# Kernel optimization log

Hardware: AMD Instinct MI355X
Metric: run time of the kernel (lower is better)

The kernel has to match this reference:

```python
import jax, jax.numpy as jnp
import numpy as np

C = 768  # in_channel == out_channel (required by conv9)

def _conv1x1(x, w, b):
    # x: [B,C,H,W], w: [O,C], b: [O]
    return jnp.einsum('bchw,oc->bohw', x, w) + b[None, :, None, None]

def _rot(x):
    # torch: gather with reversed index along dim 3, then permute(0,1,3,2)
    return jnp.swapaxes(jnp.flip(x, axis=3), 2, 3)

def _forward(hidden_states, Ws, bs):
    x = hidden_states
    B, Cc, W, H = x.shape
    o1 = _rot(x); o2 = _rot(o1); o3 = _rot(o2)
    hs11 = (jax.nn.relu(_conv1x1(x,  Ws[0], bs[0]))
          + jax.nn.relu(_conv1x1(o1, Ws[1], bs[1]))
          + jax.nn.relu(_conv1x1(o2, Ws[2], bs[2]))
          + jax.nn.relu(_conv1x1(o3, Ws[3], bs[3])))
    s = W // 2
    e1 = x[:, :, 0:s, 0:s]; e2 = x[:, :, 0:s, s:W]
    e3 = x[:, :, s:W, 0:s]; e4 = x[:, :, s:W, s:W]
    quads = [e1, e2, e3, e4]
    ts = []
    for _ in range(3):
        quads = [_rot(q) for q in quads]
        top = jnp.concatenate((quads[0], quads[1]), axis=-1)
        bot = jnp.concatenate((quads[2], quads[3]), axis=-1)
        ts.append(jnp.concatenate((top, bot), axis=-2))
    hs111 = (jax.nn.relu(_conv1x1(x,     Ws[4], bs[4]))
           + jax.nn.relu(_conv1x1(ts[0], Ws[5], bs[5]))
           + jax.nn.relu(_conv1x1(ts[1], Ws[6], bs[6]))
           + jax.nn.relu(_conv1x1(ts[2], Ws[7], bs[7])))
    # --- spatial matmul attention (per batch & channel, over HxW) ---
    q, k, v = hs11, hs111, hs11
    att = jnp.einsum('bcik,bckj->bcij', q, k)        # [B,C,W,W]
    attn = jax.nn.softmax(att, axis=-1)               # dropout = identity (eval)
    out = jnp.einsum('bcij,bcjh->bcih', attn, v)      # [B,C,W,H]
    out = jax.nn.relu(_conv1x1(out, Ws[8], bs[8]))    # proj dropout = identity (eval)
    return out

def setup_inputs() -> dict:
    key = jax.random.key(0)
    k1, k2, k3 = jax.random.split(key, 3)
    hidden_states = jax.random.normal(k1, (32, C, 32, 32), dtype=jnp.float32)
    # 9 Conv2d(C, C, kernel_size=1) layers -> stacked [9, O, C] weights and [9, O] biases
    fan_in = C
    bound = 1.0 / np.sqrt(fan_in)
    Ws = jax.random.uniform(k2, (9, C, C), minval=-bound, maxval=bound, dtype=jnp.float32)
    bs = jax.random.uniform(k3, (9, C), minval=-bound, maxval=bound, dtype=jnp.float32)
    return {"hidden_states": hidden_states, "Ws": Ws, "bs": bs}

def reference(hidden_states, Ws, bs):
    return _forward(hidden_states, Ws, bs)
```

## Files before the change

### kernel.cpp

```cpp
#include <hip/hip_runtime.h>
#include <hip/hip_fp16.h>

typedef unsigned short u16;
typedef unsigned int u32;
typedef float f32x4 __attribute__((ext_vector_type(4)));
typedef _Float16 half8 __attribute__((ext_vector_type(8)));
typedef unsigned short u16x4 __attribute__((ext_vector_type(4)));

#define CDIM 768
#define NP 1024
#define NB 32

static constexpr size_t CHW = (size_t)NB * CDIM * NP;

static constexpr size_t XT_OFF  = 0;
static constexpr size_t HS_OFF  = CHW * 2;
static constexpr size_t WHI_OFF = HS_OFF + CHW * 4;

__device__ __forceinline__ u16 f16bits(float f) {
  return __half_as_ushort(__float2half_rn(f));
}
__device__ __forceinline__ float f16tof(u16 b) {
  __half_raw hr; hr.x = b; return __half2float(__half(hr));
}
__device__ __forceinline__ u32 pk2(u32 p, float a, float b) {
  float x = f16tof((u16)(p & 0xffff)) + a;
  float y = f16tof((u16)(p >> 16)) + b;
  return (u32)f16bits(x) | ((u32)f16bits(y) << 16);
}

typedef __attribute__((address_space(1))) void gv_t;
typedef __attribute__((address_space(3))) void lv_t;
__device__ __forceinline__ void gload_lds16(const void* g, void* l) {
  __builtin_amdgcn_global_load_lds((gv_t*)g, (lv_t*)l, 16, 0, 0);
}

__global__ __launch_bounds__(256) void cast_w_k(const float* __restrict__ W,
                                                u16* __restrict__ hi) {
  int i = blockIdx.x * 256 + threadIdx.x;
  float4 v = ((const float4*)W)[i];
  u16x4 h4 = {f16bits(v.x), f16bits(v.y), f16bits(v.z), f16bits(v.w)};
  ((u16x4*)hi)[i] = h4;
}

__global__ __launch_bounds__(256) void transpose_f16_k(const float* __restrict__ src,
                                                       u16* __restrict__ dxt) {
  __shared__ float tle[32][33];
  const int b = blockIdx.z, c0 = blockIdx.y * 32, p0 = blockIdx.x * 32;
  const int tid = threadIdx.x;
  const int lr = tid >> 5, lc = tid & 31;
  const float* s = src + ((size_t)b * CDIM + c0) * NP + p0;
#pragma unroll
  for (int it = 0; it < 4; ++it) {
    int c = it * 8 + lr;
    tle[c][lc] = s[(size_t)c * NP + lc];
  }
  __syncthreads();
#pragma unroll
  for (int it = 0; it < 4; ++it) {
    int p = it * 8 + lr;
    float v = tle[lc][p];
    size_t off = ((size_t)b * NP + p0 + p) * CDIM + c0 + lc;
    dxt[off] = f16bits(v);
  }
}

__device__ __forceinline__ int sigma_fn(int mode, int z, int t, int p) {
  if (t == 0 || mode == 1) return p;
  int i = p >> 5, j = p & 31;
  if (z == 0) {
    if (t == 1) return (j << 5) | (31 - i);
    if (t == 2) return ((31 - i) << 5) | (31 - j);
    return ((31 - j) << 5) | i;
  } else {
    int ib = i & 16, jb = j & 16, il = i & 15, jl = j & 15;
    if (t == 1) return ((ib | jl) << 5) | (jb | (15 - il));
    if (t == 2) return ((ib | (15 - il)) << 5) | (jb | (15 - jl));
    return ((ib | (15 - jl)) << 5) | (jb | il);
  }
}

template <int OUTF16, int NTERMS>
__global__ __launch_bounds__(512, 2) void gemm_r(
    const u16* __restrict__ Whi,
    const u16* __restrict__ Bx,
    const float* __restrict__ bias, void* __restrict__ dst,
    int wselBase, int mode) {
  extern __shared__ u16 lds[];
  const int tid = threadIdx.x;
  const int lane = tid & 63;
  const int w = tid >> 6;
  const int wr = w >> 2, wc = w & 3;
  const int z = blockIdx.z;
  const int b = blockIdx.x >> 2;
  const int p0 = (blockIdx.x & 3) << 8;
  const int o0 = blockIdx.y << 8;
  const int l15 = lane & 15, l4 = lane >> 4;
  float* blds = (float*)(lds + 49152);
  const int NSTEP = NTERMS * 24;

  const int rA = wr * 128 + l15;
  const int baseA = rA * 32 + (l4 ^ ((rA >> 1) & 3)) * 8;
  const int rB = wc * 64 + l15;
  const int baseB = 8192 + rB * 32 + (l4 ^ ((rB >> 1) & 3)) * 8;

  int srow[2], scof[2];
#pragma unroll
  for (int it = 0; it < 2; ++it) {
    int d = it * 512 + tid;
    srow[it] = d >> 2;
    scof[it] = ((d & 3) ^ ((srow[it] >> 1) & 3)) * 8;
  }
  const u16* aptr[2];
  const u16* bptr[2];
  auto setPtrs = [&](int term) {
    int wsel = wselBase + z * 4 + term;
#pragma unroll
    for (int it = 0; it < 2; ++it) {
      aptr[it] = Whi + ((size_t)wsel * CDIM + o0 + srow[it]) * CDIM + scof[it];
      int srw = sigma_fn(mode, z, term, p0 + srow[it]);
      bptr[it] = Bx + ((size_t)b * NP + srw) * CDIM + scof[it];
    }
  };
  auto stageA = [&](u16* ldst) {
    gload_lds16(aptr[0], ldst + tid * 8);
    gload_lds16(aptr[1], ldst + 4096 + tid * 8);
    aptr[0] += 32; aptr[1] += 32;
  };
  auto stageB = [&](u16* ldst) {
    gload_lds16(bptr[0], ldst + 8192 + tid * 8);
    gload_lds16(bptr[1], ldst + 12288 + tid * 8);
    bptr[0] += 32; bptr[1] += 32;
  };

  for (int i = tid; i < NTERMS * 256; i += 512)
    blds[i] = bias[(size_t)(wselBase + z * 4 + (i >> 8)) * CDIM + o0 + (i & 255)];
  asm volatile("s_waitcnt lgkmcnt(0)" ::: "memory");

  f32x4 acc[8][4];
#pragma unroll
  for (int mi = 0; mi < 8; ++mi)
#pragma unroll
    for (int ni = 0; ni < 4; ++ni) acc[mi][ni] = (f32x4){0.f, 0.f, 0.f, 0.f};
  u32 rp[8][4][2];
  if (NTERMS > 1) {
#pragma unroll
    for (int mi = 0; mi < 8; ++mi)
#pragma unroll
      for (int ni = 0; ni < 4; ++ni) { rp[mi][ni][0] = 0u; rp[mi][ni][1] = 0u; }
  }

  setPtrs(0);
  stageA(lds); stageB(lds);
  stageA(lds + 16384); stageB(lds + 16384);

  int nsk = 2, nst = 0;
  int ckk = 0, cterm = 0;
  int cur = 0, wb = 2;

  for (int s = 0; s < NSTEP; ++s) {
    if (s + 1 < NSTEP) {
      asm volatile("s_waitcnt vmcnt(4)" ::: "memory");
    } else {
      asm volatile("s_waitcnt vmcnt(0)" ::: "memory");
    }
    __builtin_amdgcn_s_barrier();
    asm volatile("" ::: "memory");

    const u16* la = lds + cur * 16384;
    u16* ldst = lds + wb * 16384;
    const bool dostage = (s + 2) < NSTEP;
    if (dostage && nsk == 24) { ++nst; nsk = 0; setPtrs(nst); }

    half8 af[4], bf[4];
#pragma unroll
    for (int n = 0; n < 4; ++n) bf[n] = *(const half8*)(la + baseB + n * 512);
#pragma unroll
    for (int m = 0; m < 4; ++m) af[m] = *(const half8*)(la + baseA + m * 512);
    if (dostage) stageA(ldst);
    asm volatile("s_waitcnt lgkmcnt(0)" ::: "memory");
    __builtin_amdgcn_s_setprio(1);
#pragma unroll
    for (int m = 0; m < 4; ++m)
#pragma unroll
      for (int n = 0; n < 4; ++n)
        acc[m][n] = __builtin_amdgcn_mfma_f32_16x16x32_f16(af[m], bf[n], acc[m][n], 0, 0, 0);
    __builtin_amdgcn_s_setprio(0);

#pragma unroll
    for (int m = 0; m < 4; ++m) af[m] = *(const half8*)(la + baseA + (4 + m) * 512);
    if (dostage) { stageB(ldst); ++nsk; }
    asm volatile("s_waitcnt lgkmcnt(0)" ::: "memory");
    __builtin_amdgcn_s_setprio(1);
#pragma unroll
    for (int m = 0; m < 4; ++m)
#pragma unroll
      for (int n = 0; n < 4; ++n)
        acc[4 + m][n] = __builtin_amdgcn_mfma_f32_16x16x32_f16(af[m], bf[n], acc[4 + m][n], 0, 0, 0);
    __builtin_amdgcn_s_setprio(0);

    if (NTERMS > 1 && ckk == 23) {
#pragma unroll
      for (int mi = 0; mi < 8; ++mi) {
        float4 bv = *(const float4*)&blds[cterm * 256 + wr * 128 + mi * 16 + l4 * 4];
#pragma unroll
        for (int ni = 0; ni < 4; ++ni) {
          rp[mi][ni][0] = pk2(rp[mi][ni][0], fmaxf(0.f, acc[mi][ni][0] + bv.x),
                                             fmaxf(0.f, acc[mi][ni][1] + bv.y));
          rp[mi][ni][1] = pk2(rp[mi][ni][1], fmaxf(0.f, acc[mi][ni][2] + bv.z),
                                             fmaxf(0.f, acc[mi][ni][3] + bv.w));
          acc[mi][ni] = (f32x4){0.f, 0.f, 0.f, 0.f};
        }
      }
    }
    cur = cur == 2 ? 0 : cur + 1;
    wb = wb == 2 ? 0 : wb + 1;
    ++ckk; if (ckk == 24) { ckk = 0; ++cterm; }
  }

#pragma unroll
  for (int mi = 0; mi < 8; ++mi) {
    int rowb = o0 + wr * 128 + mi * 16 + l4 * 4;
#pragma unroll
    for (int ni = 0; ni < 4; ++ni) {
      int col = p0 + wc * 64 + ni * 16 + l15;
      size_t base = ((size_t)b * CDIM + rowb) * NP + col;
      if (NTERMS > 1) {
        u16* dp = (u16*)dst + (size_t)z * CHW + base;
        dp[0 * NP] = (u16)(rp[mi][ni][0] & 0xffff);
        dp[1 * NP] = (u16)(rp[mi][ni][0] >> 16);
        dp[2 * NP] = (u16)(rp[mi][ni][1] & 0xffff);
        dp[3 * NP] = (u16)(rp[mi][ni][1] >> 16);
      } else {
        float4 bv = *(const float4*)&blds[wr * 128 + mi * 16 + l4 * 4];
        float bvf[4] = {bv.x, bv.y, bv.z, bv.w};
        float* dp = (float*)dst + (size_t)z * CHW + base;
#pragma unroll
        for (int r = 0; r < 4; ++r)
          dp[(size_t)r * NP] = fmaxf(0.f, acc[mi][ni][r] + bvf[r]);
      }
    }
  }
}

__global__ __launch_bounds__(256) void attn_m_k(const u16* __restrict__ hs, u16* __restrict__ aoT) {
  __shared__ float q[4][1024];
  __shared__ float kk[4][1024];
  const int tid = threadIdx.x, w = tid >> 6, lane = tid & 63;
  const int pair0 = blockIdx.x * 4;
  const int b = pair0 / CDIM;
  const int c0 = pair0 % CDIM;
  const int l15 = lane & 15, l4 = lane >> 4;

#pragma unroll
  for (int it = 0; it < 8; ++it) {
    int d4 = it * 256 + tid;
    int pr = d4 >> 9;
    int mat = (d4 >> 8) & 1;
    int off4 = d4 & 255;
    ushort4 hv = *(const ushort4*)&hs[(size_t)mat * CHW + (size_t)(pair0 + pr) * NP + off4 * 4];
    float* dl = mat ? kk[pr] : q[pr];
    int off = off4 * 4;
    int row = off >> 5;
    int ph = ((off & 31) >> 2) ^ (row & 7) ^ (row >> 3);
    float4 v = {f16tof(hv.x), f16tof(hv.y), f16tof(hv.z), f16tof(hv.w)};
    *(float4*)&dl[row * 32 + ph * 4] = v;
  }
  __syncthreads();

  const float* Q = q[w];
  float* KK = kk[w];

  auto rd_row8 = [&](const float* M, int row) -> half8 {
    int rx = (row & 7) ^ (row >> 3);
    float4 a = *(const float4*)&M[row * 32 + ((2 * l4) ^ rx) * 4];
    float4 c = *(const float4*)&M[row * 32 + ((2 * l4 + 1) ^ rx) * 4];
    half8 h;
    h[0] = (_Float16)a.x; h[1] = (_Float16)a.y; h[2] = (_Float16)a.z; h[3] = (_Float16)a.w;
    h[4] = (_Float16)c.x; h[5] = (_Float16)c.y; h[6] = (_Float16)c.z; h[7] = (_Float16)c.w;
    return h;
  };
  auto rd_col8 = [&](const float* M, int col) -> half8 {
    half8 h;
#pragma unroll
    for (int e = 0; e < 8; ++e) {
      int row = l4 * 8 + e;
      int ph = (col >> 2) ^ (row & 7) ^ (row >> 3);
      h[e] = (_Float16)M[row * 32 + ph * 4 + (col & 3)];
    }
    return h;
  };

  half8 bq[2], akk[2];
#pragma unroll
  for (int it = 0; it < 2; ++it) bq[it] = rd_row8(Q, it * 16 + l15);
#pragma unroll
  for (int mh = 0; mh < 2; ++mh) akk[mh] = rd_col8(KK, mh * 16 + l15);
  f32x4 sacc[2][2];
#pragma unroll
  for (int mh = 0; mh < 2; ++mh)
#pragma unroll
    for (int it = 0; it < 2; ++it)
      sacc[mh][it] = __builtin_amdgcn_mfma_f32_16x16x32_f16(
          akk[mh], bq[it], (f32x4){0.f, 0.f, 0.f, 0.f}, 0, 0, 0);

#pragma unroll
  for (int it = 0; it < 2; ++it) {
    float mx = sacc[0][it][0];
#pragma unroll
    for (int r = 1; r < 4; ++r) mx = fmaxf(mx, sacc[0][it][r]);
#pragma unroll
    for (int r = 0; r < 4; ++r) mx = fmaxf(mx, sacc[1][it][r]);
    mx = fmaxf(mx, __shfl_xor(mx, 16));
    mx = fmaxf(mx, __shfl_xor(mx, 32));
    float pv[2][4];
    float sum = 0.f;
#pragma unroll
    for (int mh = 0; mh < 2; ++mh)
#pragma unroll
      for (int r = 0; r < 4; ++r) {
        pv[mh][r] = expf(sacc[mh][it][r] - mx);
        sum += pv[mh][r];
      }
    sum += __shfl_xor(sum, 16);
    sum += __shfl_xor(sum, 32);
    float inv = 1.f / sum;
    int row = it * 16 + l15;
    int rx = (row & 7) ^ (row >> 3);
#pragma unroll
    for (int mh = 0; mh < 2; ++mh) {
      float4 v = {pv[mh][0] * inv, pv[mh][1] * inv, pv[mh][2] * inv, pv[mh][3] * inv};
      *(float4*)&KK[row * 32 + ((mh * 4 + l4) ^ rx) * 4] = v;
    }
  }

  half8 bp[2], av[2];
#pragma unroll
  for (int it = 0; it < 2; ++it) bp[it] = rd_row8(KK, it * 16 + l15);
#pragma unroll
  for (int ht = 0; ht < 2; ++ht) av[ht] = rd_col8(Q, ht * 16 + l15);
  f32x4 oacc[2][2];
#pragma unroll
  for (int ht = 0; ht < 2; ++ht)
#pragma unroll
    for (int it = 0; it < 2; ++it)
      oacc[ht][it] = __builtin_amdgcn_mfma_f32_16x16x32_f16(
          av[ht], bp[it], (f32x4){0.f, 0.f, 0.f, 0.f}, 0, 0, 0);

#pragma unroll
  for (int it = 0; it < 2; ++it) {
    int row = it * 16 + l15;
    int rx = (row & 7) ^ (row >> 3);
#pragma unroll
    for (int ht = 0; ht < 2; ++ht) {
      float4 v = {oacc[ht][it][0], oacc[ht][it][1], oacc[ht][it][2], oacc[ht][it][3]};
      *(float4*)&KK[row * 32 + ((ht * 4 + l4) ^ rx) * 4] = v;
    }
  }
  __syncthreads();

#pragma unroll
  for (int it = 0; it < 4; ++it) {
    int p = it * 256 + tid;
    int row = p >> 5, col = p & 31;
    int idx = row * 32 + (((col >> 2) ^ (row & 7) ^ (row >> 3)) * 4) + (col & 3);
    ushort4 v;
    v.x = f16bits(kk[0][idx]);
    v.y = f16bits(kk[1][idx]);
    v.z = f16bits(kk[2][idx]);
    v.w = f16bits(kk[3][idx]);
    *(ushort4*)&aoT[((size_t)b * NP + p) * CDIM + c0] = v;
  }
}

extern "C" void kernel_launch(void* const* d_in, const int* in_sizes, int n_in,
                              void* d_out, int out_size, void* d_ws, size_t ws_size,
                              hipStream_t stream) {
  (void)in_sizes; (void)n_in; (void)out_size; (void)ws_size;
  const float* x = (const float*)d_in[0];
  const float* Ws = (const float*)d_in[1];
  const float* bs = (const float*)d_in[2];
  float* out = (float*)d_out;
  char* ws = (char*)d_ws;

  u16* XT  = (u16*)(ws + XT_OFF);
  u16* hs  = (u16*)(ws + HS_OFF);
  u16* Whi = (u16*)(ws + WHI_OFF);
  u16* aoT = (u16*)(ws + XT_OFF);

  cast_w_k<<<5184, 256, 0, stream>>>(Ws, Whi);
  transpose_f16_k<<<dim3(32, 24, 32), 256, 0, stream>>>(x, XT);
  gemm_r<1, 4><<<dim3(128, 3, 2), 512, 102400, stream>>>(Whi, XT, bs, (void*)hs, 0, 0);
  attn_m_k<<<6144, 256, 0, stream>>>(hs, aoT);
  gemm_r<0, 1><<<dim3(128, 3, 1), 512, 99328, stream>>>(Whi, aoT, bs, (void*)out, 8, 1);
}
```

Measured before the change: 503.9 us.

## Tile attention output layout, split GEMM main loop into four phases, store attention in f16

The attention kernel now processes 16 channel pairs per 1024-thread block. It loads Q/K directly into LDS as f16 through global_load_lds with an XOR swizzle, keeps the intermediates in f16, and writes its output in a 16-channel tiled layout. The final projection GEMM reads that tiled layout through a new template flag, giving contiguous B loads. The GEMM main loop is also split into four MFMA sub-phases, each with its own barrier and a single staged async load, to interleave copies with compute. The extra barriers per k-step could add synchronization stalls.

```diff
diff --git a/kernel.cpp b/kernel.cpp
--- a/kernel.cpp
+++ b/kernel.cpp
@@ -11,7 +11,8 @@
 #define NP 1024
 #define NB 32
 
-static constexpr size_t CHW = (size_t)NB * CDIM * NP;
+static constexpr size_t PBATCH = (size_t)CDIM * NP;
+static constexpr size_t CHW = (size_t)NB * PBATCH;
 
 static constexpr size_t XT_OFF  = 0;
 static constexpr size_t HS_OFF  = CHW * 2;
@@ -23,6 +24,7 @@
 __device__ __forceinline__ float f16tof(u16 b) {
   __half_raw hr; hr.x = b; return __half2float(__half(hr));
 }
+__device__ __forceinline__ int akey(int r) { return ((r >> 1) & 3) ^ ((r >> 3) & 3); }
 __device__ __forceinline__ u32 pk2(u32 p, float a, float b) {
   float x = f16tof((u16)(p & 0xffff)) + a;
   float y = f16tof((u16)(p >> 16)) + b;
@@ -80,8 +82,8 @@
   }
 }
 
-template <int OUTF16, int NTERMS>
-__global__ __launch_bounds__(512, 2) void gemm_r(
+template <int OUTF16, int NTERMS, int TILEDB>
+__global__ __launch_bounds__(512, 2) void gemm_q8(
     const u16* __restrict__ Whi,
     const u16* __restrict__ Bx,
     const float* __restrict__ bias, void* __restrict__ dst,
@@ -118,19 +120,20 @@
 #pragma unroll
     for (int it = 0; it < 2; ++it) {
       aptr[it] = Whi + ((size_t)wsel * CDIM + o0 + srow[it]) * CDIM + scof[it];
-      int srw = sigma_fn(mode, z, term, p0 + srow[it]);
-      bptr[it] = Bx + ((size_t)b * NP + srw) * CDIM + scof[it];
+      if (TILEDB) {
+        int cc = scof[it];
+        bptr[it] = Bx + (size_t)b * PBATCH + (size_t)(cc >> 4) * (NP * 16) +
+                   (size_t)(p0 + srow[it]) * 16 + (cc & 15);
+      } else {
+        int srw = sigma_fn(mode, z, term, p0 + srow[it]);
+        bptr[it] = Bx + ((size_t)b * NP + srw) * CDIM + scof[it];
+      }
     }
   };
-  auto stageA = [&](u16* ldst) {
-    gload_lds16(aptr[0], ldst + tid * 8);
-    gload_lds16(aptr[1], ldst + 4096 + tid * 8);
+  auto advPtrs = [&]() {
     aptr[0] += 32; aptr[1] += 32;
-  };
-  auto stageB = [&](u16* ldst) {
-    gload_lds16(bptr[0], ldst + 8192 + tid * 8);
-    gload_lds16(bptr[1], ldst + 12288 + tid * 8);
-    bptr[0] += 32; bptr[1] += 32;
+    if (TILEDB) { bptr[0] += 32768; bptr[1] += 32768; }
+    else { bptr[0] += 32; bptr[1] += 32; }
   };
 
   for (int i = tid; i < NTERMS * 256; i += 512)
@@ -151,8 +154,16 @@
   }
 
   setPtrs(0);
-  stageA(lds); stageB(lds);
-  stageA(lds + 16384); stageB(lds + 16384);
+  gload_lds16(aptr[0], lds + tid * 8);
+  gload_lds16(aptr[1], lds + 4096 + tid * 8);
+  gload_lds16(bptr[0], lds + 8192 + tid * 8);
+  gload_lds16(bptr[1], lds + 12288 + tid * 8);
+  advPtrs();
+  gload_lds16(aptr[0], lds + 16384 + tid * 8);
+  gload_lds16(aptr[1], lds + 16384 + 4096 + tid * 8);
+  gload_lds16(bptr[0], lds + 16384 + 8192 + tid * 8);
+  gload_lds16(bptr[1], lds + 16384 + 12288 + tid * 8);
+  advPtrs();
 
   int nsk = 2, nst = 0;
   int ckk = 0, cterm = 0;
@@ -170,33 +181,65 @@
     const u16* la = lds + cur * 16384;
     u16* ldst = lds + wb * 16384;
     const bool dostage = (s + 2) < NSTEP;
-    if (dostage && nsk == 24) { ++nst; nsk = 0; setPtrs(nst); }
-
-    half8 af[4], bf[4];
+    if (NTERMS > 1 && dostage && nsk == 24) { ++nst; nsk = 0; setPtrs(nst); }
+
+    half8 bf[4], af[2];
 #pragma unroll
     for (int n = 0; n < 4; ++n) bf[n] = *(const half8*)(la + baseB + n * 512);
-#pragma unroll
-    for (int m = 0; m < 4; ++m) af[m] = *(const half8*)(la + baseA + m * 512);
-    if (dostage) stageA(ldst);
+    af[0] = *(const half8*)(la + baseA);
+    af[1] = *(const half8*)(la + baseA + 512);
+    if (dostage) gload_lds16(aptr[0], ldst + tid * 8);
+    __builtin_amdgcn_s_barrier();
     asm volatile("s_waitcnt lgkmcnt(0)" ::: "memory");
     __builtin_amdgcn_s_setprio(1);
 #pragma unroll
-    for (int m = 0; m < 4; ++m)
-#pragma unroll
-      for (int n = 0; n < 4; ++n)
-        acc[m][n] = __builtin_amdgcn_mfma_f32_16x16x32_f16(af[m], bf[n], acc[m][n], 0, 0, 0);
+    for (int n = 0; n < 4; ++n) {
+      acc[0][n] = __builtin_amdgcn_mfma_f32_16x16x32_f16(af[0], bf[n], acc[0][n], 0, 0, 0);
+      acc[1][n] = __builtin_amdgcn_mfma_f32_16x16x32_f16(af[1], bf[n], acc[1][n], 0, 0, 0);
+    }
     __builtin_amdgcn_s_setprio(0);
 
-#pragma unroll
-    for (int m = 0; m < 4; ++m) af[m] = *(const half8*)(la + baseA + (4 + m) * 512);
-    if (dostage) { stageB(ldst); ++nsk; }
+    af[0] = *(const half8*)(la + baseA + 2 * 512);
+    af[1] = *(const half8*)(la + baseA + 3 * 512);
+    if (dostage) gload_lds16(aptr[1], ldst + 4096 + tid * 8);
+    __builtin_amdgcn_s_barrier();
     asm volatile("s_waitcnt lgkmcnt(0)" ::: "memory");
     __builtin_amdgcn_s_setprio(1);
 #pragma unroll
-    for (int m = 0; m < 4; ++m)
-#pragma unroll
-      for (int n = 0; n < 4; ++n)
-        acc[4 + m][n] = __builtin_amdgcn_mfma_f32_16x16x32_f16(af[m], bf[n], acc[4 + m][n], 0, 0, 0);
+    for (int n = 0; n < 4; ++n) {
+      acc[2][n] = __builtin_amdgcn_mfma_f32_16x16x32_f16(af[0], bf[n], acc[2][n], 0, 0, 0);
+      acc[3][n] = __builtin_amdgcn_mfma_f32_16x16x32_f16(af[1], bf[n], acc[3][n], 0, 0, 0);
+    }
+    __builtin_amdgcn_s_setprio(0);
+
+    af[0] = *(const half8*)(la + baseA + 4 * 512);
+    af[1] = *(const half8*)(la + baseA + 5 * 512);
+    if (dostage) gload_lds16(bptr[0], ldst + 8192 + tid * 8);
+    __builtin_amdgcn_s_barrier();
+    asm volatile("s_waitcnt lgkmcnt(0)" ::: "memory");
+    __builtin_amdgcn_s_setprio(1);
+#pragma unroll
+    for (int n = 0; n < 4; ++n) {
+      acc[4][n] = __builtin_amdgcn_mfma_f32_16x16x32_f16(af[0], bf[n], acc[4][n], 0, 0, 0);
+      acc[5][n] = __builtin_amdgcn_mfma_f32_16x16x32_f16(af[1], bf[n], acc[5][n], 0, 0, 0);
+    }
+    __builtin_amdgcn_s_setprio(0);
+
+    af[0] = *(const half8*)(la + baseA + 6 * 512);
+    af[1] = *(const half8*)(la + baseA + 7 * 512);
+    if (dostage) {
+      gload_lds16(bptr[1], ldst + 12288 + tid * 8);
+      advPtrs();
+      ++nsk;
+    }
+    __builtin_amdgcn_s_barrier();
+    asm volatile("s_waitcnt lgkmcnt(0)" ::: "memory");
+    __builtin_amdgcn_s_setprio(1);
+#pragma unroll
+    for (int n = 0; n < 4; ++n) {
+      acc[6][n] = __builtin_amdgcn_mfma_f32_16x16x32_f16(af[0], bf[n], acc[6][n], 0, 0, 0);
+      acc[7][n] = __builtin_amdgcn_mfma_f32_16x16x32_f16(af[1], bf[n], acc[7][n], 0, 0, 0);
+    }
     __builtin_amdgcn_s_setprio(0);
 
     if (NTERMS > 1 && ckk == 23) {
@@ -243,59 +286,47 @@
   }
 }
 
-__global__ __launch_bounds__(256) void attn_m_k(const u16* __restrict__ hs, u16* __restrict__ aoT) {
-  __shared__ float q[4][1024];
-  __shared__ float kk[4][1024];
+__global__ __launch_bounds__(1024) void attn_t_k(const u16* __restrict__ hs, u16* __restrict__ aoT) {
+  extern __shared__ u16 att[];
   const int tid = threadIdx.x, w = tid >> 6, lane = tid & 63;
-  const int pair0 = blockIdx.x * 4;
+  const int pair0 = blockIdx.x * 16;
   const int b = pair0 / CDIM;
   const int c0 = pair0 % CDIM;
   const int l15 = lane & 15, l4 = lane >> 4;
 
 #pragma unroll
-  for (int it = 0; it < 8; ++it) {
-    int d4 = it * 256 + tid;
-    int pr = d4 >> 9;
-    int mat = (d4 >> 8) & 1;
-    int off4 = d4 & 255;
-    ushort4 hv = *(const ushort4*)&hs[(size_t)mat * CHW + (size_t)(pair0 + pr) * NP + off4 * 4];
-    float* dl = mat ? kk[pr] : q[pr];
-    int off = off4 * 4;
-    int row = off >> 5;
-    int ph = ((off & 31) >> 2) ^ (row & 7) ^ (row >> 3);
-    float4 v = {f16tof(hv.x), f16tof(hv.y), f16tof(hv.z), f16tof(hv.w)};
-    *(float4*)&dl[row * 32 + ph * 4] = v;
-  }
+  for (int it = 0; it < 4; ++it) {
+    int d = it * 1024 + tid;
+    int pair = d >> 8, mat = (d >> 7) & 1, rem = d & 127;
+    int r = rem >> 2, ph = rem & 3;
+    int ch = ph ^ akey(r);
+    const u16* src = hs + (size_t)mat * CHW + (size_t)(pair0 + pair) * NP + r * 32 + ch * 8;
+    gload_lds16(src, att + (size_t)d * 8);
+  }
+  asm volatile("s_waitcnt vmcnt(0)" ::: "memory");
   __syncthreads();
 
-  const float* Q = q[w];
-  float* KK = kk[w];
-
-  auto rd_row8 = [&](const float* M, int row) -> half8 {
-    int rx = (row & 7) ^ (row >> 3);
-    float4 a = *(const float4*)&M[row * 32 + ((2 * l4) ^ rx) * 4];
-    float4 c = *(const float4*)&M[row * 32 + ((2 * l4 + 1) ^ rx) * 4];
-    half8 h;
-    h[0] = (_Float16)a.x; h[1] = (_Float16)a.y; h[2] = (_Float16)a.z; h[3] = (_Float16)a.w;
-    h[4] = (_Float16)c.x; h[5] = (_Float16)c.y; h[6] = (_Float16)c.z; h[7] = (_Float16)c.w;
-    return h;
+  u16* Qb = att + w * 2048;
+  u16* Kb = Qb + 1024;
+
+  auto rd_row8 = [&](const u16* M, int row) -> half8 {
+    return *(const half8*)(M + row * 32 + (l4 ^ akey(row)) * 8);
   };
-  auto rd_col8 = [&](const float* M, int col) -> half8 {
-    half8 h;
+  auto rd_col8 = [&](const u16* M, int col) -> half8 {
+    union { u16 u[8]; half8 h; } t;
 #pragma unroll
     for (int e = 0; e < 8; ++e) {
       int row = l4 * 8 + e;
-      int ph = (col >> 2) ^ (row & 7) ^ (row >> 3);
-      h[e] = (_Float16)M[row * 32 + ph * 4 + (col & 3)];
-    }
-    return h;
+      t.u[e] = M[row * 32 + ((col >> 3) ^ akey(row)) * 8 + (col & 7)];
+    }
+    return t.h;
   };
 
   half8 bq[2], akk[2];
 #pragma unroll
-  for (int it = 0; it < 2; ++it) bq[it] = rd_row8(Q, it * 16 + l15);
-#pragma unroll
-  for (int mh = 0; mh < 2; ++mh) akk[mh] = rd_col8(KK, mh * 16 + l15);
+  for (int it = 0; it < 2; ++it) bq[it] = rd_row8(Qb, it * 16 + l15);
+#pragma unroll
+  for (int mh = 0; mh < 2; ++mh) akk[mh] = rd_col8(Kb, mh * 16 + l15);
   f32x4 sacc[2][2];
 #pragma unroll
   for (int mh = 0; mh < 2; ++mh)
@@ -326,19 +357,22 @@
     sum += __shfl_xor(sum, 32);
     float inv = 1.f / sum;
     int row = it * 16 + l15;
-    int rx = (row & 7) ^ (row >> 3);
+    int rk = akey(row);
 #pragma unroll
     for (int mh = 0; mh < 2; ++mh) {
-      float4 v = {pv[mh][0] * inv, pv[mh][1] * inv, pv[mh][2] * inv, pv[mh][3] * inv};
-      *(float4*)&KK[row * 32 + ((mh * 4 + l4) ^ rx) * 4] = v;
+      int c = mh * 16 + l4 * 4;
+      uint2 wv;
+      wv.x = (u32)f16bits(pv[mh][0] * inv) | ((u32)f16bits(pv[mh][1] * inv) << 16);
+      wv.y = (u32)f16bits(pv[mh][2] * inv) | ((u32)f16bits(pv[mh][3] * inv) << 16);
+      *(uint2*)(Kb + row * 32 + ((c >> 3) ^ rk) * 8 + (c & 7)) = wv;
     }
   }
 
   half8 bp[2], av[2];
 #pragma unroll
-  for (int it = 0; it < 2; ++it) bp[it] = rd_row8(KK, it * 16 + l15);
-#pragma unroll
-  for (int ht = 0; ht < 2; ++ht) av[ht] = rd_col8(Q, ht * 16 + l15);
+  for (int it = 0; it < 2; ++it) bp[it] = rd_row8(Kb, it * 16 + l15);
+#pragma unroll
+  for (int ht = 0; ht < 2; ++ht) av[ht] = rd_col8(Qb, ht * 16 + l15);
   f32x4 oacc[2][2];
 #pragma unroll
   for (int ht = 0; ht < 2; ++ht)
@@ -350,26 +384,30 @@
 #pragma unroll
   for (int it = 0; it < 2; ++it) {
     int row = it * 16 + l15;
-    int rx = (row & 7) ^ (row >> 3);
+    int rk = akey(row);
 #pragma unroll
     for (int ht = 0; ht < 2; ++ht) {
-      float4 v = {oacc[ht][it][0], oacc[ht][it][1], oacc[ht][it][2], oacc[ht][it][3]};
-      *(float4*)&KK[row * 32 + ((ht * 4 + l4) ^ rx) * 4] = v;
+      int c = ht * 16 + l4 * 4;
+      uint2 wv;
+      wv.x = (u32)f16bits(oacc[ht][it][0]) | ((u32)f16bits(oacc[ht][it][1]) << 16);
+      wv.y = (u32)f16bits(oacc[ht][it][2]) | ((u32)f16bits(oacc[ht][it][3]) << 16);
+      *(uint2*)(Qb + row * 32 + ((c >> 3) ^ rk) * 8 + (c & 7)) = wv;
     }
   }
   __syncthreads();
 
 #pragma unroll
   for (int it = 0; it < 4; ++it) {
-    int p = it * 256 + tid;
-    int row = p >> 5, col = p & 31;
-    int idx = row * 32 + (((col >> 2) ^ (row & 7) ^ (row >> 3)) * 4) + (col & 3);
+    int s = it * 1024 + tid;
+    int p = s >> 2, cq = s & 3;
+    int row = p >> 5, colh = p & 31;
+    int boff = row * 32 + ((colh >> 3) ^ akey(row)) * 8 + (colh & 7);
     ushort4 v;
-    v.x = f16bits(kk[0][idx]);
-    v.y = f16bits(kk[1][idx]);
-    v.z = f16bits(kk[2][idx]);
-    v.w = f16bits(kk[3][idx]);
-    *(ushort4*)&aoT[((size_t)b * NP + p) * CDIM + c0] = v;
+    v.x = att[(cq * 4 + 0) * 2048 + boff];
+    v.y = att[(cq * 4 + 1) * 2048 + boff];
+    v.z = att[(cq * 4 + 2) * 2048 + boff];
+    v.w = att[(cq * 4 + 3) * 2048 + boff];
+    *(ushort4*)&aoT[(size_t)b * PBATCH + (size_t)(c0 >> 4) * (NP * 16) + (size_t)p * 16 + cq * 4] = v;
   }
 }
 
@@ -390,7 +428,7 @@
 
   cast_w_k<<<5184, 256, 0, stream>>>(Ws, Whi);
   transpose_f16_k<<<dim3(32, 24, 32), 256, 0, stream>>>(x, XT);
-  gemm_r<1, 4><<<dim3(128, 3, 2), 512, 102400, stream>>>(Whi, XT, bs, (void*)hs, 0, 0);
-  attn_m_k<<<6144, 256, 0, stream>>>(hs, aoT);
-  gemm_r<0, 1><<<dim3(128, 3, 1), 512, 99328, stream>>>(Whi, aoT, bs, (void*)out, 8, 1);
-}
+  gemm_q8<1, 4, 0><<<dim3(128, 3, 2), 512, 102400, stream>>>(Whi, XT, bs, (void*)hs, 0, 0);
+  attn_t_k<<<1536, 1024, 65536, stream>>>(hs, aoT);
+  gemm_q8<0, 1, 1><<<dim3(128, 3, 1), 512, 99328, stream>>>(Whi, aoT, bs, (void*)out, 8, 1);
+}
```

Result: faster. 443.6 us (-12.0%).
